# Performance work log

Measured on AMD Instinct MI355X. Metric: run time of the kernel, lower is better.

Reference implementation:

```python
import jax, jax.numpy as jnp
import numpy as np

B, N, DESC, H, MAXK = 32, 2048, 16, 64, 2
P = DESC + H            # concat feature dim
KMAT = 2 * MAXK + 1     # num diffusion matrices (identity + MAXK per support)


def setup_inputs() -> dict:
    key = jax.random.key(0)
    ks = jax.random.split(key, 8)
    return {
        "inputs": jax.random.normal(ks[0], (B, N * DESC), jnp.float32),
        "state": jax.random.normal(ks[1], (B, N * H), jnp.float32),
        "adj": jax.random.uniform(ks[2], (N, N), jnp.float32),
        "theta_r": jax.random.normal(ks[3], (P * KMAT, H), jnp.float32) * 0.05,
        "theta_u": jax.random.normal(ks[4], (P * KMAT, H), jnp.float32) * 0.05,
        "theta_c": jax.random.normal(ks[5], (P * KMAT, H), jnp.float32) * 0.05,
        "bias_r": jnp.zeros((1, H), jnp.float32),
        "bias_u": jnp.zeros((1, H), jnp.float32),
        "bias_c": jnp.zeros((1, H), jnp.float32),
    }


def _random_walk_T(adj):
    # transpose(D^-1 A): row-normalize then transpose
    d = jnp.sum(adj, axis=1, keepdims=True)
    d_inv = jnp.where(d > 0, 1.0 / d, 0.0)
    return (d_inv * adj).T  # [N, N]


def _gconv(x_in, h, supports, theta, bias):
    # x_in: [B, N*DESC], h: [B, N*H]
    x = jnp.concatenate(
        [x_in.reshape(B, N, DESC), h.reshape(B, N, H)], axis=-1
    )  # [B, N, P]
    xs = [x]
    for S in supports:
        xk = x
        for _ in range(MAXK):  # pure powers S^k x, as in the source
            xk = jnp.einsum("mn,bnp->bmp", S, xk)
            xs.append(xk)
    all_x = jnp.stack(xs, axis=-1)  # [B, N, P, KMAT]
    out = all_x.reshape(B * N, P * KMAT) @ theta + bias  # [B*N, H]
    return out.reshape(B, N * H)


def reference(inputs, state, adj, theta_r, theta_u, theta_c, bias_r, bias_u, bias_c):
    supports = (_random_walk_T(adj), _random_walk_T(adj.T))
    r = jax.nn.sigmoid(_gconv(inputs, state, supports, theta_r, bias_r))
    u = jax.nn.sigmoid(_gconv(inputs, state, supports, theta_u, bias_u))
    c = jnp.tanh(_gconv(inputs, r * state, supports, theta_c, bias_c))
    return u * state + (1.0 - u) * c  # [B, N*H]
```

## Files before the change

kernel.cpp:

```cpp
#include <hip/hip_runtime.h>
#include <hip/hip_bf16.h>

#define Bb    32
#define Nn_   2048
#define DESCn 16
#define Hn    64
#define Pn    80
#define KM    5

#define XSTRIDE ((size_t)Bb * Pn * Nn_)

typedef __attribute__((ext_vector_type(8))) short bf16x8;
typedef __attribute__((ext_vector_type(4))) short s16x4;
typedef __attribute__((ext_vector_type(4))) float f32x4;

__device__ __forceinline__ short f2bf(float f) {
    unsigned u = __builtin_bit_cast(unsigned, f);
    u = u + 0x7FFFu + ((u >> 16) & 1u);
    return (short)(u >> 16);
}
__device__ __forceinline__ float bf2f(short s) {
    unsigned u = ((unsigned)(unsigned short)s) << 16;
    return __builtin_bit_cast(float, u);
}

__device__ __forceinline__ void glds16(const void* g, void* l) {
    __builtin_amdgcn_global_load_lds((const __attribute__((address_space(1))) void*)g,
                                     (__attribute__((address_space(3))) void*)l, 16, 0, 0);
}


__global__ void sums_kernel(const float* __restrict__ adj, float* __restrict__ rsum,
                            float* __restrict__ csum) {
    __shared__ float tile[64][65];
    const int r0 = blockIdx.y * 64, c0 = blockIdx.x * 64;
    const int t = threadIdx.x;
    for (int i = t; i < 64 * 64; i += 256)
        tile[i >> 6][i & 63] = adj[(size_t)(r0 + (i >> 6)) * Nn_ + c0 + (i & 63)];
    __syncthreads();
    if (t < 64) {
        float s = 0.f;
#pragma unroll 8
        for (int j = 0; j < 64; ++j) s += tile[t][j];
        atomicAdd(&rsum[r0 + t], s);
    } else if (t < 128) {
        int c = t - 64;
        float s = 0.f;
#pragma unroll 8
        for (int j = 0; j < 64; ++j) s += tile[j][c];
        atomicAdd(&csum[c0 + c], s);
    }
}

__global__ void inv2_kernel(const float* __restrict__ rs, const float* __restrict__ cs,
                            float* __restrict__ ri, float* __restrict__ ci) {
    int i = blockIdx.x * 256 + threadIdx.x;
    if (i < Nn_) {
        ri[i] = rs[i] > 0.f ? 1.f / rs[i] : 0.f;
        ci[i] = cs[i] > 0.f ? 1.f / cs[i] : 0.f;
    }
}

__global__ void build_S_kernel(const float* __restrict__ adj, const float* __restrict__ rinv,
                               const float* __restrict__ cinv, short* __restrict__ S0,
                               short* __restrict__ S1, short* __restrict__ S0T,
                               short* __restrict__ S1T) {
    __shared__ float tile[64][65];
    int r0 = blockIdx.y * 64, c0 = blockIdx.x * 64;
    for (int i = threadIdx.x; i < 64 * 64; i += 256) {
        int r = i >> 6, c = i & 63;
        float a = adj[(size_t)(r0 + r) * Nn_ + c0 + c];
        size_t o = (size_t)(r0 + r) * Nn_ + c0 + c;
        S1[o]  = f2bf(a * cinv[c0 + c]);
        S0T[o] = f2bf(a * rinv[r0 + r]);
    }
    for (int i = threadIdx.x; i < 64 * 64; i += 256) {
        int a = i >> 6, b = i & 63;
        tile[a][b] = adj[(size_t)(c0 + a) * Nn_ + r0 + b];
    }
    __syncthreads();
    for (int i = threadIdx.x; i < 64 * 64; i += 256) {
        int r = i >> 6, c = i & 63;
        float at = tile[c][r];
        size_t o = (size_t)(r0 + r) * Nn_ + c0 + c;
        S0[o]  = f2bf(at * rinv[c0 + c]);
        S1T[o] = f2bf(at * cinv[r0 + r]);
    }
}


__global__ void build_x0_kernel(const float* __restrict__ inputs, const float* __restrict__ state,
                                short* __restrict__ x0) {
    const int b = blockIdx.y, n0 = blockIdx.x * 64;
    __shared__ float sIn[64][17];
    __shared__ float sSt[64][65];
    const int t = threadIdx.x;
    const float* ip = inputs + ((size_t)b * Nn_ + n0) * DESCn;
    for (int i = t; i < 64 * DESCn; i += 256) sIn[i >> 4][i & 15] = ip[i];
    const float* sp = state + ((size_t)b * Nn_ + n0) * Hn;
    for (int i = t; i < 64 * Hn; i += 256) sSt[i >> 6][i & 63] = sp[i];
    __syncthreads();
    for (int i = t; i < Pn * 64; i += 256) {
        int pp = i >> 6, nn = i & 63;
        float v = (pp < DESCn) ? sIn[nn][pp] : sSt[nn][pp - DESCn];
        x0[((size_t)pp * Bb + b) * Nn_ + n0 + nn] = f2bf(v);
    }
}

__global__ void reorder_theta3_kernel(const float* __restrict__ thR, const float* __restrict__ thU,
                                      const float* __restrict__ thC, short* __restrict__ TR,
                                      short* __restrict__ TU, short* __restrict__ TC) {
    int i = blockIdx.x * 256 + threadIdx.x;
    if (i >= KM * 64 * 96) return;
    int k = i / (64 * 96);
    int rem = i % (64 * 96);
    int h = rem / 96, pp = rem % 96;
    if (pp < Pn) {
        size_t idx = ((size_t)pp * KM + k) * Hn + h;
        TR[i] = f2bf(thR[idx]);
        TU[i] = f2bf(thU[idx]);
        TC[i] = f2bf(thC[idx]);
    } else {
        TR[i] = 0; TU[i] = 0; TC[i] = 0;
    }
}


struct GemmJob  { const short* A; const short* B; short* D; int yStart; };
struct GemmJobs { GemmJob j[4]; };

#define MMAQ(RH, CH, RB)                                                        \
    {                                                                           \
        __builtin_amdgcn_s_setprio(1);                                          \
        _Pragma("unroll")                                                       \
        for (int ks = 0; ks < 2; ++ks)                                          \
            _Pragma("unroll")                                                   \
            for (int fm = 0; fm < 4; ++fm)                                      \
                _Pragma("unroll")                                               \
                for (int fn = 0; fn < 2; ++fn)                                  \
                    acc[RH][CH][fm][fn] = __builtin_amdgcn_mfma_f32_16x16x32_bf16( \
                        rA[fm][ks], RB[fn][ks], acc[RH][CH][fm][fn], 0, 0, 0);  \
        __builtin_amdgcn_s_setprio(0);                                          \
    }

#define LOADA(D_, RH)                                                           \
    _Pragma("unroll")                                                           \
    for (int fm = 0; fm < 4; ++fm)                                              \
        _Pragma("unroll")                                                       \
        for (int ks = 0; ks < 2; ++ks)                                          \
            rA[fm][ks] = readA(D_, RH, fm, ks);

#define LOADB(D_, CH, RB)                                                       \
    _Pragma("unroll")                                                           \
    for (int fn = 0; fn < 2; ++fn)                                              \
        _Pragma("unroll")                                                       \
        for (int ks = 0; ks < 2; ++ks)                                          \
            RB[fn][ks] = readB(D_, CH, fn, ks);

#define SYNCW()                                                   \
    asm volatile("s_waitcnt lgkmcnt(0)" ::: "memory");            \
    __builtin_amdgcn_sched_barrier(0);                            \
    __builtin_amdgcn_s_barrier();                                 \
    __builtin_amdgcn_sched_barrier(0);

#define SYNCWV()                                                  \
    asm volatile("s_waitcnt lgkmcnt(0)" ::: "memory");            \
    __builtin_amdgcn_sched_barrier(0);                            \
    asm volatile("s_waitcnt vmcnt(4)" ::: "memory");              \
    __builtin_amdgcn_s_barrier();                                 \
    __builtin_amdgcn_sched_barrier(0);

__global__ __launch_bounds__(512, 2)
void gemm_bt_256(GemmJobs jobs, int nJobs, int K, int NN) {
    __shared__ __align__(16) short lds[65536];

    const int by = blockIdx.y;
    int jsel = 0;
#pragma unroll
    for (int q = 1; q < 4; ++q)
        if (q < nJobs && by >= jobs.j[q].yStart) jsel = q;
    const GemmJob jb = jobs.j[jsel];
    const short* __restrict__ A  = jb.A;
    const short* __restrict__ Bm = jb.B;
    short* __restrict__ D = jb.D;

    const int c0 = (by - jb.yStart) * 256;
    const int m0 = blockIdx.x * 256;
    const int tid = threadIdx.x;
    const int w = tid >> 6, lane = tid & 63;
    const int wm = w >> 2, wn = w & 3;
    const int l16 = lane & 15, g = lane >> 4;
    const int swz = l16 & 7;

    const int srow = tid >> 3;
    const int scol = ((tid & 7) ^ (srow & 7)) * 8;
    const int stOff = w * 512;

    const short* Abase = A + (size_t)c0 * K;
    const short* Bbase = Bm + (size_t)m0 * K;

    auto stageA = [&](int h, int t) {
        const short* gb = Abase + (size_t)(h * 128) * K + t * 64 + scol;
        short* lb = lds + ((t & 1) * 16384 + h * 8192) + stOff;
#pragma unroll
        for (int i = 0; i < 2; ++i)
            glds16(gb + (size_t)(i * 64 + srow) * K, lb + i * 4096);
    };
    auto stageB = [&](int h, int t) {
        const short* gb = Bbase + (size_t)(h * 128) * K + t * 64 + scol;
        short* lb = lds + (32768 + (t & 1) * 16384 + h * 8192) + stOff;
#pragma unroll
        for (int i = 0; i < 2; ++i)
            glds16(gb + (size_t)(i * 64 + srow) * K, lb + i * 4096);
    };

    auto readA = [&](int d, int rh, int fm, int ks) -> bf16x8 {
        int r7 = rh * 64 + fm * 16 + l16;
        int idx = d * 16384 + wm * 8192 + r7 * 64 + (((ks * 4 + g) ^ swz) * 8);
        return *(const bf16x8*)(lds + idx);
    };
    auto readB = [&](int d, int ch, int fn, int ks) -> bf16x8 {
        int r7 = (wn & 1) * 64 + ch * 32 + fn * 16 + l16;
        int idx = 32768 + d * 16384 + (wn >> 1) * 8192 + r7 * 64 + (((ks * 4 + g) ^ swz) * 8);
        return *(const bf16x8*)(lds + idx);
    };

    f32x4 acc[2][2][4][2];
    const f32x4 fz = {0.f, 0.f, 0.f, 0.f};
#pragma unroll
    for (int a = 0; a < 2; ++a)
#pragma unroll
        for (int b = 0; b < 2; ++b)
#pragma unroll
            for (int c = 0; c < 4; ++c)
#pragma unroll
                for (int d = 0; d < 2; ++d) acc[a][b][c][d] = fz;

    bf16x8 rA[4][2], rB0[2][2], rB1[2][2];

    const int KS = K >> 6;
    const int J  = KS >> 1;

    stageA(0, 0); stageA(1, 0); stageB(0, 0); stageB(1, 0);
    stageB(0, 1); stageB(1, 1);
    asm volatile("s_waitcnt vmcnt(4)" ::: "memory");
    __builtin_amdgcn_s_barrier();
    __builtin_amdgcn_sched_barrier(0);

    LOADA(0, 0);
    LOADB(0, 0, rB0);
    LOADB(0, 1, rB1);
    stageA(0, 1); stageA(1, 1);
    SYNCW();

#pragma unroll 1
    for (int j = 0; j < J; ++j) {
        const int tn0 = (2 * j + 2 < KS) ? 2 * j + 2 : KS - 1;
        const int tn1 = (2 * j + 3 < KS) ? 2 * j + 3 : KS - 1;

        MMAQ(0, 0, rB0);
        MMAQ(0, 1, rB1);
        LOADA(0, 1);
        stageB(0, tn0); stageB(1, tn0);
        SYNCWV();
        MMAQ(1, 1, rB1);
        MMAQ(1, 0, rB0);
        LOADA(1, 0);
        LOADB(1, 0, rB0);
        LOADB(1, 1, rB1);
        stageA(0, tn0); stageA(1, tn0);
        SYNCW();
        MMAQ(0, 0, rB0);
        MMAQ(0, 1, rB1);
        LOADA(1, 1);
        stageB(0, tn1); stageB(1, tn1);
        SYNCWV();
        MMAQ(1, 1, rB1);
        MMAQ(1, 0, rB0);
        if (j + 1 < J) {
            LOADA(0, 0);
            LOADB(0, 0, rB0);
            LOADB(0, 1, rB1);
            stageA(0, tn1); stageA(1, tn1);
        }
        SYNCW();
    }

    asm volatile("s_waitcnt vmcnt(0)" ::: "memory");
    __syncthreads();
    float* tb = (float*)lds + w * 1088;
#pragma unroll
    for (int rh = 0; rh < 2; ++rh)
#pragma unroll
        for (int fm = 0; fm < 4; ++fm) {
#pragma unroll
            for (int ch = 0; ch < 2; ++ch)
#pragma unroll
                for (int fn = 0; fn < 2; ++fn) {
                    f32x4 v = acc[rh][ch][fm][fn];
#pragma unroll
                    for (int r = 0; r < 4; ++r)
                        tb[(g * 4 + r) * 68 + ch * 32 + fn * 16 + l16] = v[r];
                }
            const int crow0 = c0 + wm * 128 + rh * 64 + fm * 16;
            const int mcol = m0 + wn * 64 + lane;
#pragma unroll
            for (int rr = 0; rr < 16; ++rr)
                D[(size_t)(crow0 + rr) * NN + mcol] = f2bf(tb[rr * 68 + lane]);
        }
}


__global__ __launch_bounds__(256, 2)
void theta_ru_kernel(const short* __restrict__ X, const short* __restrict__ ThR,
                     const short* __restrict__ ThU, const float* __restrict__ biasR,
                     const float* __restrict__ biasU, const float* __restrict__ state,
                     short* __restrict__ Uout, short* __restrict__ x0) {
    __shared__ short ldsAr[64 * 40];
    __shared__ short ldsAu[64 * 40];
    __shared__ short ldsB[32 * 136];
    const int b = blockIdx.y, n0 = blockIdx.x * 128;
    const int t = threadIdx.x, w = t >> 6, lane = t & 63;
    const int l16 = lane & 15, g = lane >> 4;
    const f32x4 fz = {0.f, 0.f, 0.f, 0.f};
    const bf16x8 bz = {0, 0, 0, 0, 0, 0, 0, 0};

    f32x4 aR[4][2], aU[4][2];
#pragma unroll
    for (int i = 0; i < 4; i++)
#pragma unroll
        for (int j = 0; j < 2; j++) { aR[i][j] = fz; aU[i][j] = fz; }

    const int hA = t >> 2, pcA = (t & 3) * 8;

    for (int kb = 0; kb < KM; kb++) {
        for (int ks = 0; ks < 3; ks++) {
            __syncthreads();
            *(bf16x8*)(ldsAr + hA * 40 + pcA) =
                *(const bf16x8*)(ThR + ((size_t)kb * 64 + hA) * 96 + ks * 32 + pcA);
            *(bf16x8*)(ldsAu + hA * 40 + pcA) =
                *(const bf16x8*)(ThU + ((size_t)kb * 64 + hA) * 96 + ks * 32 + pcA);
#pragma unroll
            for (int i = 0; i < 2; i++) {
                int q = t + i * 256;
                int pp = q >> 4, nc = (q & 15) * 8;
                int pg = ks * 32 + pp;
                bf16x8 v = bz;
                if (pg < Pn)
                    v = *(const bf16x8*)(X + (size_t)kb * XSTRIDE + ((size_t)pg * Bb + b) * Nn_ + n0 + nc);
                *(bf16x8*)(ldsB + pp * 136 + nc) = v;
            }
            __syncthreads();
            bf16x8 ar[4], au[4];
#pragma unroll
            for (int mi = 0; mi < 4; mi++) {
                int hr = mi * 16 + l16;
                ar[mi] = *(const bf16x8*)(ldsAr + hr * 40 + g * 8);
                au[mi] = *(const bf16x8*)(ldsAu + hr * 40 + g * 8);
            }
#pragma unroll
            for (int nj = 0; nj < 2; nj++) {
                int col = w * 32 + nj * 16 + l16;
                bf16x8 bv;
#pragma unroll
                for (int j = 0; j < 8; j++) bv[j] = ldsB[(g * 8 + j) * 136 + col];
#pragma unroll
                for (int mi = 0; mi < 4; mi++) {
                    aR[mi][nj] = __builtin_amdgcn_mfma_f32_16x16x32_bf16(ar[mi], bv, aR[mi][nj], 0, 0, 0);
                    aU[mi][nj] = __builtin_amdgcn_mfma_f32_16x16x32_bf16(au[mi], bv, aU[mi][nj], 0, 0, 0);
                }
            }
        }
    }
#pragma unroll
    for (int mi = 0; mi < 4; mi++)
#pragma unroll
        for (int nj = 0; nj < 2; nj++) {
            int n = n0 + w * 32 + nj * 16 + l16;
            int h0 = mi * 16 + g * 4;
            size_t base = ((size_t)b * Nn_ + n) * Hn + h0;
            f32x4 st = *(const f32x4*)(state + base);
            s16x4 uv;
#pragma unroll
            for (int r = 0; r < 4; r++) {
                float zr = aR[mi][nj][r] + biasR[h0 + r];
                float zu = aU[mi][nj][r] + biasU[h0 + r];
                float rr = 1.f / (1.f + __expf(-zr));
                uv[r] = f2bf(1.f / (1.f + __expf(-zu)));
                x0[((size_t)(DESCn + h0 + r) * Bb + b) * Nn_ + n] = f2bf(rr * st[r]);
            }
            *(s16x4*)(Uout + base) = uv;
        }
}

__global__ __launch_bounds__(256, 2)
void theta_c_kernel(const short* __restrict__ X, const short* __restrict__ ThC,
                    const float* __restrict__ biasC, const short* __restrict__ U,
                    const float* __restrict__ state, float* __restrict__ out) {
    __shared__ short ldsA[64 * 40];
    __shared__ short ldsB[32 * 136];
    const int b = blockIdx.y, n0 = blockIdx.x * 128;
    const int t = threadIdx.x, w = t >> 6, lane = t & 63;
    const int l16 = lane & 15, g = lane >> 4;
    const f32x4 fz = {0.f, 0.f, 0.f, 0.f};
    const bf16x8 bz = {0, 0, 0, 0, 0, 0, 0, 0};

    f32x4 aC[4][2];
#pragma unroll
    for (int i = 0; i < 4; i++)
#pragma unroll
        for (int j = 0; j < 2; j++) aC[i][j] = fz;

    const int hA = t >> 2, pcA = (t & 3) * 8;

    for (int kb = 0; kb < KM; kb++) {
        for (int ks = 0; ks < 3; ks++) {
            __syncthreads();
            *(bf16x8*)(ldsA + hA * 40 + pcA) =
                *(const bf16x8*)(ThC + ((size_t)kb * 64 + hA) * 96 + ks * 32 + pcA);
#pragma unroll
            for (int i = 0; i < 2; i++) {
                int q = t + i * 256;
                int pp = q >> 4, nc = (q & 15) * 8;
                int pg = ks * 32 + pp;
                bf16x8 v = bz;
                if (pg < Pn)
                    v = *(const bf16x8*)(X + (size_t)kb * XSTRIDE + ((size_t)pg * Bb + b) * Nn_ + n0 + nc);
                *(bf16x8*)(ldsB + pp * 136 + nc) = v;
            }
            __syncthreads();
            bf16x8 ac[4];
#pragma unroll
            for (int mi = 0; mi < 4; mi++)
                ac[mi] = *(const bf16x8*)(ldsA + (mi * 16 + l16) * 40 + g * 8);
#pragma unroll
            for (int nj = 0; nj < 2; nj++) {
                int col = w * 32 + nj * 16 + l16;
                bf16x8 bv;
#pragma unroll
                for (int j = 0; j < 8; j++) bv[j] = ldsB[(g * 8 + j) * 136 + col];
#pragma unroll
                for (int mi = 0; mi < 4; mi++)
                    aC[mi][nj] = __builtin_amdgcn_mfma_f32_16x16x32_bf16(ac[mi], bv, aC[mi][nj], 0, 0, 0);
            }
        }
    }
#pragma unroll
    for (int mi = 0; mi < 4; mi++)
#pragma unroll
        for (int nj = 0; nj < 2; nj++) {
            int n = n0 + w * 32 + nj * 16 + l16;
            int h0 = mi * 16 + g * 4;
            size_t base = ((size_t)b * Nn_ + n) * Hn + h0;
            f32x4 st = *(const f32x4*)(state + base);
            s16x4 uv = *(const s16x4*)(U + base);
            f32x4 o;
#pragma unroll
            for (int r = 0; r < 4; r++) {
                float cc = tanhf(aC[mi][nj][r] + biasC[h0 + r]);
                float uu = bf2f(uv[r]);
                o[r] = uu * st[r] + (1.f - uu) * cc;
            }
            *(f32x4*)(out + base) = o;
        }
}


extern "C" void kernel_launch(void* const* d_in, const int* in_sizes, int n_in,
                              void* d_out, int out_size, void* d_ws, size_t ws_size,
                              hipStream_t stream) {
    (void)in_sizes; (void)n_in; (void)out_size; (void)ws_size;
    const float* inputs = (const float*)d_in[0];
    const float* state  = (const float*)d_in[1];
    const float* adj    = (const float*)d_in[2];
    const float* thR    = (const float*)d_in[3];
    const float* thU    = (const float*)d_in[4];
    const float* thC    = (const float*)d_in[5];
    const float* bR     = (const float*)d_in[6];
    const float* bU     = (const float*)d_in[7];
    const float* bC     = (const float*)d_in[8];
    float* out = (float*)d_out;

    char* p = (char*)d_ws;
    auto alloc = [&](size_t bytes) -> void* {
        void* r = (void*)p;
        p += (bytes + 255) & ~(size_t)255;
        return r;
    };
    short* S0   = (short*)alloc((size_t)Nn_ * Nn_ * 2);
    short* S1   = (short*)alloc((size_t)Nn_ * Nn_ * 2);
    short* Ssq0 = (short*)alloc((size_t)Nn_ * Nn_ * 2);
    short* Ssq1 = (short*)alloc((size_t)Nn_ * Nn_ * 2);
    float* rinv = (float*)alloc(Nn_ * 4);
    float* cinv = (float*)alloc(Nn_ * 4);
    float* sums = (float*)alloc(2 * Nn_ * 4);
    short* xb   = (short*)alloc(5 * XSTRIDE * 2);
    short* TR   = (short*)alloc((size_t)KM * 64 * 96 * 2);
    short* TU   = (short*)alloc((size_t)KM * 64 * 96 * 2);
    short* TC   = (short*)alloc((size_t)KM * 64 * 96 * 2);
    short* Ub   = (short*)alloc((size_t)Bb * Nn_ * Hn * 2);

    short* x0 = xb;
    short* y1 = xb + 1 * XSTRIDE;
    short* y2 = xb + 2 * XSTRIDE;
    short* y3 = xb + 3 * XSTRIDE;
    short* y4 = xb + 4 * XSTRIDE;
    short* S0T = y3;
    short* S1T = y4;
    const size_t HOFF = (size_t)DESCn * Bb * Nn_;

    hipMemsetAsync(sums, 0, 2 * Nn_ * 4, stream);
    sums_kernel<<<dim3(32, 32), 256, 0, stream>>>(adj, sums, sums + Nn_);
    inv2_kernel<<<Nn_ / 256, 256, 0, stream>>>(sums, sums + Nn_, rinv, cinv);
    build_S_kernel<<<dim3(32, 32), 256, 0, stream>>>(adj, rinv, cinv, S0, S1, S0T, S1T);
    build_x0_kernel<<<dim3(32, Bb), 256, 0, stream>>>(inputs, state, x0);
    int rt_grid = (KM * 64 * 96 + 255) / 256;
    reorder_theta3_kernel<<<rt_grid, 256, 0, stream>>>(thR, thU, thC, TR, TU, TC);

    GemmJobs d1;
    d1.j[0] = { S0, S0T, Ssq0, 0 };
    d1.j[1] = { S1, S1T, Ssq1, 8 };
    d1.j[2] = { x0, S0,   y1, 16 };
    d1.j[3] = d1.j[2];
    gemm_bt_256<<<dim3(8, 26), 512, 0, stream>>>(d1, 3, Nn_, Nn_);

    GemmJobs d2;
    d2.j[0] = { x0, S1,   y3, 0 };
    d2.j[1] = { x0, Ssq0, y2, 10 };
    d2.j[2] = { x0, Ssq1, y4, 20 };
    d2.j[3] = d2.j[2];
    gemm_bt_256<<<dim3(8, 30), 512, 0, stream>>>(d2, 3, Nn_, Nn_);

    theta_ru_kernel<<<dim3(Nn_ / 128, Bb), 256, 0, stream>>>(xb, TR, TU, bR, bU, state, Ub, x0);

    GemmJobs d3;
    d3.j[0] = { x0 + HOFF, S0,   y1 + HOFF, 0 };
    d3.j[1] = { x0 + HOFF, Ssq0, y2 + HOFF, 8 };
    d3.j[2] = { x0 + HOFF, S1,   y3 + HOFF, 16 };
    d3.j[3] = { x0 + HOFF, Ssq1, y4 + HOFF, 24 };
    gemm_bt_256<<<dim3(8, 32), 512, 0, stream>>>(d3, 4, Nn_, Nn_);

    theta_c_kernel<<<dim3(Nn_ / 128, Bb), 256, 0, stream>>>(xb, TC, bC, Ub, state, out);
}
```

Before: 258.6 us.

## Stagger MFMA phases across wave roles and vectorize bf16 epilogue stores

Splits the waves into two roles so that half of them issue their MFMA blocks before each barrier and the other half after it. The aim is to interleave matrix work with the LDS loads and global staging across waves, so the matrix units are not idle at sync points. The epilogue now packs eight bf16 values per lane and writes them with one 16-byte store instead of scalar 2-byte stores. The staggered schedule relies on the existing barriers still protecting the register and LDS buffers for both roles, which is easy to get wrong.

```diff
diff --git a/kernel.cpp b/kernel.cpp
--- a/kernel.cpp
+++ b/kernel.cpp
@@ -191,6 +191,7 @@
     const int wm = w >> 2, wn = w & 3;
     const int l16 = lane & 15, g = lane >> 4;
     const int swz = l16 & 7;
+    const int role = (w ^ (w >> 2)) & 1;
 
     const int srow = tid >> 3;
     const int scol = ((tid & 7) ^ (srow & 7)) * 8;
@@ -251,6 +252,7 @@
     LOADB(0, 0, rB0);
     LOADB(0, 1, rB1);
     stageA(0, 1); stageA(1, 1);
+    if (role == 0) { MMAQ(0, 0, rB0); MMAQ(0, 1, rB1); }
     SYNCW();
 
 #pragma unroll 1
@@ -258,30 +260,30 @@
         const int tn0 = (2 * j + 2 < KS) ? 2 * j + 2 : KS - 1;
         const int tn1 = (2 * j + 3 < KS) ? 2 * j + 3 : KS - 1;
 
-        MMAQ(0, 0, rB0);
-        MMAQ(0, 1, rB1);
+        if (role) { MMAQ(0, 0, rB0); MMAQ(0, 1, rB1); }
         LOADA(0, 1);
         stageB(0, tn0); stageB(1, tn0);
+        if (!role) { MMAQ(1, 1, rB1); MMAQ(1, 0, rB0); }
         SYNCWV();
-        MMAQ(1, 1, rB1);
-        MMAQ(1, 0, rB0);
+        if (role) { MMAQ(1, 1, rB1); MMAQ(1, 0, rB0); }
         LOADA(1, 0);
         LOADB(1, 0, rB0);
         LOADB(1, 1, rB1);
         stageA(0, tn0); stageA(1, tn0);
+        if (!role) { MMAQ(0, 0, rB0); MMAQ(0, 1, rB1); }
         SYNCW();
-        MMAQ(0, 0, rB0);
-        MMAQ(0, 1, rB1);
+        if (role) { MMAQ(0, 0, rB0); MMAQ(0, 1, rB1); }
         LOADA(1, 1);
         stageB(0, tn1); stageB(1, tn1);
+        if (!role) { MMAQ(1, 1, rB1); MMAQ(1, 0, rB0); }
         SYNCWV();
-        MMAQ(1, 1, rB1);
-        MMAQ(1, 0, rB0);
+        if (role) { MMAQ(1, 1, rB1); MMAQ(1, 0, rB0); }
         if (j + 1 < J) {
             LOADA(0, 0);
             LOADB(0, 0, rB0);
             LOADB(0, 1, rB1);
             stageA(0, tn1); stageA(1, tn1);
+            if (!role) { MMAQ(0, 0, rB0); MMAQ(0, 1, rB1); }
         }
         SYNCW();
     }
@@ -289,6 +291,8 @@
     asm volatile("s_waitcnt vmcnt(0)" ::: "memory");
     __syncthreads();
     float* tb = (float*)lds + w * 1088;
+    const int r8 = lane >> 3;
+    const int cg = (lane & 7) * 8;
 #pragma unroll
     for (int rh = 0; rh < 2; ++rh)
 #pragma unroll
@@ -303,10 +307,15 @@
                         tb[(g * 4 + r) * 68 + ch * 32 + fn * 16 + l16] = v[r];
                 }
             const int crow0 = c0 + wm * 128 + rh * 64 + fm * 16;
-            const int mcol = m0 + wn * 64 + lane;
-#pragma unroll
-            for (int rr = 0; rr < 16; ++rr)
-                D[(size_t)(crow0 + rr) * NN + mcol] = f2bf(tb[rr * 68 + lane]);
+            const int mbase = m0 + wn * 64 + cg;
+#pragma unroll
+            for (int ii = 0; ii < 2; ++ii) {
+                int row = ii * 8 + r8;
+                bf16x8 pk;
+#pragma unroll
+                for (int jj = 0; jj < 8; ++jj) pk[jj] = f2bf(tb[row * 68 + cg + jj]);
+                *(bf16x8*)(D + (size_t)(crow0 + row) * NN + mbase) = pk;
+            }
         }
 }
 
```

Measured after the change: 249.7 us. 3.4% less time.
